# Optimization experiments

Measured on AMD Instinct MI355X. Metric: run time of the kernel, lower is better.

The kernel has to match this reference:

```python
import jax, jax.numpy as jnp
import numpy as np

M_FUZZ = 2.0        # self.m
EPSILON = 1e-8      # self.Epsilon
MAX_ITER = 25       # self.max_iterion


def setup_inputs() -> dict:
    key = jax.random.key(0)
    k1, k2 = jax.random.split(key)
    data = jax.random.normal(k1, (300000, 64), dtype=jnp.float32)
    u0_raw = jax.random.uniform(k2, (300000, 64), dtype=jnp.float32)
    return {"data": data, "u0_raw": u0_raw, "cluster": 64}


def reference(data, u0_raw, cluster):
    # Fuzzy c-means, faithful to GranularComputing.forward:
    #   iterate: C = center(U); U = update(U, C); C_new = center(U);
    #            stop if ||C_new - C||_F < Epsilon; return C (pre-update center).
    m = M_FUZZ
    p = 2.0 / (m - 1.0)  # exponent in membership update (== 2.0)
    N, D = data.shape

    # initialize_matrix_U: random rows normalized to sum to 1
    U0 = u0_raw / jnp.sum(u0_raw, axis=1, keepdims=True)  # [N, c]

    def center(U):
        Um = U ** m                                        # [N, c]
        num = Um.T @ data                                  # [c, D]
        den = jnp.sum(Um, axis=0)[:, None]                 # [c, 1]
        return num / den

    x2 = jnp.sum(data * data, axis=1, keepdims=True)       # [N, 1]

    def sqdist(C):
        # squared Euclidean distances [N, c] via expansion (no N x c x D tensor)
        c2 = jnp.sum(C * C, axis=1)                        # [c]
        return jnp.maximum(x2 + c2 - 2.0 * (data @ C.T), 0.0)

    def step(carry, _):
        U, C_ret, done = carry
        C = center(U)                                      # [c, D]
        # u_ij = 1 / sum_k (d_ij / d_ik)^p  ==  d_ij^{-p} / sum_k d_ik^{-p}
        w = sqdist(C) ** (-p / 2.0)                        # [N, c]
        U_new = w / jnp.sum(w, axis=1, keepdims=True)
        C_new = center(U_new)
        diff = jnp.sqrt(jnp.sum((C_new - C) ** 2))
        # freeze state after convergence (emulates the early break)
        U_out = jnp.where(done, U, U_new)
        C_out = jnp.where(done, C_ret, C)
        return (U_out, C_out, done | (diff < EPSILON)), None

    C0 = jnp.zeros((cluster, D), dtype=data.dtype)
    (_, V, _), _ = jax.lax.scan(
        step, (U0, C0, jnp.array(False)), None, length=MAX_ITER + 1
    )
    return V  # [cluster, D]
```

## Files before the change

### kernel.cpp

```cpp
#include <hip/hip_runtime.h>


#define DM 64
#define CL 64
#define PARTIAL_STRIDE 4160
#define MAX_ITER 25
#define MAX_BLOCKS 768
#define LDP 72

typedef __attribute__((ext_vector_type(8))) short bf16x8;
typedef __attribute__((ext_vector_type(4))) float f32x4;

__device__ __forceinline__ unsigned f2bf1(float f) {
  unsigned u = __builtin_bit_cast(unsigned, f);
  return (u + 0x7FFFu + ((u >> 16) & 1u)) >> 16;
}
__device__ __forceinline__ unsigned pkbf(float a, float b) {
  return f2bf1(a) | (f2bf1(b) << 16);
}
__device__ __forceinline__ unsigned cvtpk_bf16(float a, float b) {
  unsigned r;
  asm("v_cvt_pk_bf16_f32 %0, %1, %2" : "=v"(r) : "v"(a), "v"(b));
  return r;
}

__device__ __forceinline__ float wave_sum(float v) {
#define DPPADD(ctrl, rmask)                                                  \
  v += __builtin_bit_cast(float, __builtin_amdgcn_update_dpp(                \
           0, __builtin_bit_cast(int, v), ctrl, rmask, 0xf, false));
  DPPADD(0x111, 0xf)
  DPPADD(0x112, 0xf)
  DPPADD(0x114, 0xf)
  DPPADD(0x118, 0xf)
  DPPADD(0x142, 0xa)
  DPPADD(0x143, 0xc)
#undef DPPADD
  return __builtin_bit_cast(
      float, __builtin_amdgcn_readlane(__builtin_bit_cast(int, v), 63));
}

__device__ __forceinline__ float group16_sum(float v) {
#define DPPADD(ctrl)                                                         \
  v += __builtin_bit_cast(float, __builtin_amdgcn_update_dpp(                \
           0, __builtin_bit_cast(int, v), ctrl, 0xf, 0xf, false));
  DPPADD(0xB1)
  DPPADD(0x4E)
  DPPADD(0x141)
  DPPADD(0x140)
#undef DPPADD
  return v;
}

__global__ __launch_bounds__(256)
void fcm_prep(const float* __restrict__ data, float* __restrict__ x2,
              unsigned short* __restrict__ xbf,
              float* __restrict__ diffac, int* __restrict__ done,
              int* __restrict__ ticket, int N) {
  size_t i = (size_t)blockIdx.x * blockDim.x + threadIdx.x;
  if (i == 0) { *diffac = 0.0f; *done = 0; *ticket = 0; }
  size_t nvec = (size_t)N * (DM / 4);
  if (i >= nvec) return;
  float4 v = ((const float4*)data)[i];
  float s = fmaf(v.x, v.x, fmaf(v.y, v.y, fmaf(v.z, v.z, v.w * v.w)));
  float rs = group16_sum(s);
  if ((threadIdx.x & 15) == 0) x2[i >> 4] = rs;
  uint2 pk = {cvtpk_bf16(v.x, v.y), cvtpk_bf16(v.z, v.w)};
  ((uint2*)xbf)[i] = pk;
}

template <bool INIT>
__global__ __launch_bounds__(256, 3)
void fcm_pass(const unsigned short* __restrict__ xbf, const float* __restrict__ x2,
              const float* __restrict__ CU,
              float* __restrict__ partial, const int* __restrict__ done,
              int N, int ntiles) {
  if (!INIT && *done) return;
  __shared__ __align__(16) unsigned short Xb[2][64 * LDP];
  __shared__ __align__(16) unsigned short XTb[2][64 * LDP];
  __shared__ __align__(16) unsigned short umT[64 * LDP];
  __shared__ __align__(16) float x2s[2][64];

  const int tid  = threadIdx.x;
  const int w    = __builtin_amdgcn_readfirstlane(tid >> 6);
  const int col  = tid & 15;
  const int quad = (tid >> 4) & 3;

  bf16x8 cf0[4], cf1[4];
  float c2v[4];
  if (!INIT) {
#pragma unroll
    for (int jt = 0; jt < 4; jt++) {
      const float* crow = CU + (size_t)(16 * jt + col) * DM;
      float4 ca = *(const float4*)(crow + quad * 8);
      float4 cb = *(const float4*)(crow + quad * 8 + 4);
      float4 cc = *(const float4*)(crow + 32 + quad * 8);
      float4 cd = *(const float4*)(crow + 32 + quad * 8 + 4);
      float cp = ca.x*ca.x + ca.y*ca.y + ca.z*ca.z + ca.w*ca.w
               + cb.x*cb.x + cb.y*cb.y + cb.z*cb.z + cb.w*cb.w
               + cc.x*cc.x + cc.y*cc.y + cc.z*cc.z + cc.w*cc.w
               + cd.x*cd.x + cd.y*cd.y + cd.z*cd.z + cd.w*cd.w;
      cp += __shfl_xor(cp, 16, 64);
      cp += __shfl_xor(cp, 32, 64);
      c2v[jt] = cp;
      union { bf16x8 v; unsigned u[4]; } P0, P1;
      P0.u[0] = pkbf(ca.x, ca.y); P0.u[1] = pkbf(ca.z, ca.w);
      P0.u[2] = pkbf(cb.x, cb.y); P0.u[3] = pkbf(cb.z, cb.w);
      P1.u[0] = pkbf(cc.x, cc.y); P1.u[1] = pkbf(cc.z, cc.w);
      P1.u[2] = pkbf(cd.x, cd.y); P1.u[3] = pkbf(cd.z, cd.w);
      cf0[jt] = P0.v; cf1[jt] = P1.v;
    }
  }

  union { bf16x8 v; unsigned u[4]; } ON;
  ON.u[0] = ON.u[1] = ON.u[2] = ON.u[3] = 0x3F803F80u;
  const bf16x8 onesf = ON.v;

  f32x4 D2[4];
#pragma unroll
  for (int dt = 0; dt < 4; dt++) D2[dt] = f32x4{0.f, 0.f, 0.f, 0.f};
  f32x4 Dden = f32x4{0.f, 0.f, 0.f, 0.f};

  const int sp  = tid & 63;
  const int sd0 = (tid >> 6) * 8;
  const unsigned short* gsrc = xbf + (size_t)sp * DM + sd0;

  auto do_gemm2 = [&](int cb) {
#pragma unroll
    for (int pb = 0; pb < 2; pb++) {
      bf16x8 au = *(const bf16x8*)(const void*)&umT[(16 * w + col) * LDP + pb * 32 + quad * 8];
      Dden = __builtin_amdgcn_mfma_f32_16x16x32_bf16(au, onesf, Dden, 0, 0, 0);
#pragma unroll
      for (int dt = 0; dt < 4; dt++) {
        bf16x8 bx = *(const bf16x8*)(const void*)&XTb[cb][(dt * 16 + col) * LDP + pb * 32 + quad * 8];
        D2[dt] = __builtin_amdgcn_mfma_f32_16x16x32_bf16(au, bx, D2[dt], 0, 0, 0);
      }
    }
  };

  bf16x8 rv0 = {0, 0, 0, 0, 0, 0, 0, 0};
  bf16x8 rv1 = {0, 0, 0, 0, 0, 0, 0, 0};
  float rx2 = 0.0f;
  {
    int t0 = blockIdx.x;
    if (t0 < ntiles) {
      int base = t0 * 64;
      int np = min(64, N - base);
      if (sp < np) {
        const unsigned short* g = gsrc + (size_t)base * DM;
        rv0 = *(const bf16x8*)(g);
        rv1 = *(const bf16x8*)(g + 32);
      }
      if (tid < 64 && base + tid < N) rx2 = x2[base + tid];
    }
  }

  int c = 0;
  int it = 0;
  for (int t = blockIdx.x; t < ntiles; t += gridDim.x, ++it) {
    const int base = t * 64;
    const int np = min(64, N - base);
    __syncthreads();

    if (it > 0) do_gemm2(c ^ 1);

    *(bf16x8*)(void*)&Xb[c][sp * LDP + sd0] = rv0;
    *(bf16x8*)(void*)&Xb[c][sp * LDP + sd0 + 32] = rv1;
#pragma unroll
    for (int k = 0; k < 8; k++) XTb[c][(sd0 + k) * LDP + sp] = (unsigned short)rv0[k];
#pragma unroll
    for (int k = 0; k < 8; k++) XTb[c][(sd0 + 32 + k) * LDP + sp] = (unsigned short)rv1[k];
    if (tid < 64) x2s[c][tid] = rx2;

    {
      int tn = t + gridDim.x;
      rv0 = bf16x8{0, 0, 0, 0, 0, 0, 0, 0};
      rv1 = bf16x8{0, 0, 0, 0, 0, 0, 0, 0};
      rx2 = 0.0f;
      if (tn < ntiles) {
        int nbase = tn * 64;
        int nnp = min(64, N - nbase);
        if (sp < nnp) {
          const unsigned short* g = gsrc + (size_t)nbase * DM;
          rv0 = *(const bf16x8*)(g);
          rv1 = *(const bf16x8*)(g + 32);
        }
        if (tid < 64 && nbase + tid < N) rx2 = x2[nbase + tid];
      }
    }
    __syncthreads();

    float Wv[4][4];
    if (INIT) {
#pragma unroll
      for (int jt = 0; jt < 4; jt++)
#pragma unroll
        for (int r = 0; r < 4; r++) {
          int pl = 16 * w + quad * 4 + r;
          Wv[jt][r] = (pl < np)
              ? CU[(size_t)(base + pl) * CL + 16 * jt + col] : 0.0f;
        }
    } else {
      bf16x8 a0 = *(const bf16x8*)(const void*)&Xb[c][(16 * w + col) * LDP + quad * 8];
      bf16x8 a1 = *(const bf16x8*)(const void*)&Xb[c][(16 * w + col) * LDP + 32 + quad * 8];
      f32x4 x2p = *(const f32x4*)(const void*)&x2s[c][16 * w + quad * 4];
#pragma unroll
      for (int jt = 0; jt < 4; jt++) {
        f32x4 s = f32x4{0.f, 0.f, 0.f, 0.f};
        s = __builtin_amdgcn_mfma_f32_16x16x32_bf16(a0, cf0[jt], s, 0, 0, 0);
        s = __builtin_amdgcn_mfma_f32_16x16x32_bf16(a1, cf1[jt], s, 0, 0, 0);
#pragma unroll
        for (int r = 0; r < 4; r++) {
          float dist = fmaxf(fmaf(-2.0f, s[r], x2p[r] + c2v[jt]), 0.0f);
          Wv[jt][r] = __builtin_amdgcn_rcpf(dist);
        }
      }
    }

    float rr[4];
#pragma unroll
    for (int r = 0; r < 4; r++) {
      float rs = Wv[0][r] + Wv[1][r] + Wv[2][r] + Wv[3][r];
      rs = group16_sum(rs);
      int pl = 16 * w + quad * 4 + r;
      rr[r] = (pl < np) ? __builtin_amdgcn_rcpf(rs) : 0.0f;
    }

#pragma unroll
    for (int jt = 0; jt < 4; jt++) {
      float u0v = Wv[jt][0] * rr[0], u1v = Wv[jt][1] * rr[1];
      float u2v = Wv[jt][2] * rr[2], u3v = Wv[jt][3] * rr[3];
      uint2 pk = {cvtpk_bf16(u0v * u0v, u1v * u1v),
                  cvtpk_bf16(u2v * u2v, u3v * u3v)};
      *(uint2*)(void*)&umT[(16 * jt + col) * LDP + 16 * w + quad * 4] = pk;
    }
    c ^= 1;
  }

  if (it > 0) {
    __syncthreads();
    do_gemm2(c ^ 1);
  }

  float* pbuf = partial + (size_t)blockIdx.x * PARTIAL_STRIDE;
  if (col == 0) {
    float4 dv = {Dden[0], Dden[1], Dden[2], Dden[3]};
    *(float4*)(void*)&pbuf[CL * DM + 16 * w + quad * 4] = dv;
  }
#pragma unroll
  for (int dt = 0; dt < 4; dt++)
#pragma unroll
    for (int r = 0; r < 4; r++)
      pbuf[(size_t)(16 * w + quad * 4 + r) * DM + dt * 16 + col] = D2[dt][r];
}

__global__ __launch_bounds__(1024, 1)
void fcm_reduce(const float* __restrict__ partial, float* __restrict__ Cnew,
                const float* __restrict__ Cold, float* __restrict__ out,
                float* __restrict__ diffac, int* __restrict__ done,
                int* __restrict__ ticket, int compute_diff, int nb) {
  if (compute_diff && *done) return;
  __shared__ float sm[16 * 64];
  __shared__ float sden[1024];
  __shared__ int lastflag;
  __shared__ float sdiff;
  int j = blockIdx.x;
  int tid = threadIdx.x;
  int d = tid & 63;
  int slice = tid >> 6;
  float s = 0.0f;
  for (int b = slice; b < nb; b += 16)
    s += partial[(size_t)b * PARTIAL_STRIDE + j * DM + d];
  sm[slice * 64 + d] = s;
  float dv = 0.0f;
  for (int b = tid; b < nb; b += 1024)
    dv += partial[(size_t)b * PARTIAL_STRIDE + CL * DM + j];
  sden[tid] = dv;
  __syncthreads();
#pragma unroll
  for (int st = 8; st; st >>= 1) {
    if (slice < st) sm[slice * 64 + d] += sm[(slice + st) * 64 + d];
    __syncthreads();
  }
#pragma unroll
  for (int st = 512; st >= 64; st >>= 1) {
    if (tid < st) sden[tid] += sden[tid + st];
    __syncthreads();
  }
  if (tid < 64) {
    float denj = wave_sum(sden[tid]);
    float c = sm[tid] / denj;
    Cnew[j * DM + tid] = c;
    if (compute_diff) {
      float df = c - Cold[j * DM + tid];
      float tot = wave_sum(df * df);
      if (tid == 0) atomicAdd(diffac, tot);
    }
  }
  if (!compute_diff) return;
  __syncthreads();
  if (tid == 0) {
    __threadfence();
    int t = atomicAdd(ticket, 1);
    lastflag = (t == (int)gridDim.x - 1);
  }
  __syncthreads();
  if (!lastflag) return;
  if (tid == 0) sdiff = atomicAdd(diffac, 0.0f);
  __syncthreads();
  if (sdiff < 1e-16f) {
    for (int i = tid; i < CL * DM; i += 1024) out[i] = Cold[i];
    if (tid == 0) *done = 1;
  }
  if (tid == 0) { *diffac = 0.0f; *ticket = 0; }
}

__global__ void fcm_final(const float* __restrict__ Clast, float* __restrict__ out,
                          const int* __restrict__ done) {
  if (*done) return;
  int i = blockIdx.x * blockDim.x + threadIdx.x;
  if (i < CL * DM) out[i] = Clast[i];
}

extern "C" void kernel_launch(void* const* d_in, const int* in_sizes, int n_in,
                              void* d_out, int out_size, void* d_ws, size_t ws_size,
                              hipStream_t stream) {
  const float* data = (const float*)d_in[0];
  const float* u0   = (const float*)d_in[1];
  float* out = (float*)d_out;
  int N = in_sizes[0] / DM;
  int ntiles = (N + 63) / 64;

  float* ws = (float*)d_ws;
  size_t Noff = ((size_t)N + 15) & ~(size_t)15;
  float* x2 = ws;
  unsigned short* xbf = (unsigned short*)(ws + Noff);
  float* C0 = ws + Noff + (size_t)N * 32;
  float* C1 = C0 + CL * DM;
  float* diffac = C1 + CL * DM;
  int* done = (int*)(diffac + 1);
  int* ticket = (int*)(diffac + 2);
  float* partial = diffac + 16;

  size_t used = Noff + (size_t)N * 32 + 2 * CL * DM + 16;
  size_t avail = (ws_size / 4 > used) ? (ws_size / 4 - used) / PARTIAL_STRIDE : 0;
  int nb = (int)(avail < MAX_BLOCKS ? avail : MAX_BLOCKS);
  if (nb < 1) nb = 1;

  size_t nvec = (size_t)N * (DM / 4);
  hipLaunchKernelGGL(fcm_prep, dim3((unsigned)((nvec + 255) / 256)), dim3(256), 0,
                     stream, data, x2, xbf, diffac, done, ticket, N);
  hipLaunchKernelGGL((fcm_pass<true>), dim3(nb), dim3(256), 0, stream,
                     xbf, x2, u0, partial, done, N, ntiles);
  hipLaunchKernelGGL(fcm_reduce, dim3(64), dim3(1024), 0, stream,
                     partial, C0, C1, out, diffac, done, ticket, 0, nb);

  float* bufs[2] = {C0, C1};
  for (int k = 0; k < MAX_ITER; k++) {
    float* Cc = bufs[k & 1];
    float* Cn = bufs[(k + 1) & 1];
    hipLaunchKernelGGL((fcm_pass<false>), dim3(nb), dim3(256), 0, stream,
                       xbf, x2, Cc, partial, done, N, ntiles);
    hipLaunchKernelGGL(fcm_reduce, dim3(64), dim3(1024), 0, stream,
                       partial, Cn, Cc, out, diffac, done, ticket, 1, nb);
  }
  hipLaunchKernelGGL(fcm_final, dim3(16), dim3(256), 0, stream,
                     bufs[1], out, done);
}
```

Before: 379.0 us.

## Fuse per-iteration center reduction into the pass kernel with a grid spin barrier

```diff
diff --git a/kernel.cpp b/kernel.cpp
--- a/kernel.cpp
+++ b/kernel.cpp
@@ -55,9 +55,9 @@
 void fcm_prep(const float* __restrict__ data, float* __restrict__ x2,
               unsigned short* __restrict__ xbf,
               float* __restrict__ diffac, int* __restrict__ done,
-              int* __restrict__ ticket, int N) {
+              int* __restrict__ ticket, int* __restrict__ rdone, int N) {
   size_t i = (size_t)blockIdx.x * blockDim.x + threadIdx.x;
-  if (i == 0) { *diffac = 0.0f; *done = 0; *ticket = 0; }
+  if (i == 0) { *diffac = 0.0f; *done = 0; *ticket = 0; *rdone = 0; }
   size_t nvec = (size_t)N * (DM / 4);
   if (i >= nvec) return;
   float4 v = ((const float4*)data)[i];
@@ -68,74 +68,156 @@
   ((uint2*)xbf)[i] = pk;
 }
 
-template <bool INIT>
 __global__ __launch_bounds__(256, 3)
-void fcm_pass(const unsigned short* __restrict__ xbf, const float* __restrict__ x2,
-              const float* __restrict__ CU,
-              float* __restrict__ partial, const int* __restrict__ done,
-              int N, int ntiles) {
-  if (!INIT && *done) return;
+void fcm_pass_init(const unsigned short* __restrict__ xbf,
+                   const float* __restrict__ CU,
+                   float* __restrict__ partial, int N, int ntiles) {
+  __shared__ __align__(16) unsigned short Xb[2][64 * LDP];
+  __shared__ __align__(16) unsigned short XTb[2][64 * LDP];
+  __shared__ __align__(16) unsigned short umT[64 * LDP];
+
+  const int tid  = threadIdx.x;
+  const int w    = __builtin_amdgcn_readfirstlane(tid >> 6);
+  const int col  = tid & 15;
+  const int quad = (tid >> 4) & 3;
+
+  union { bf16x8 v; unsigned u[4]; } ON;
+  ON.u[0] = ON.u[1] = ON.u[2] = ON.u[3] = 0x3F803F80u;
+  const bf16x8 onesf = ON.v;
+
+  f32x4 D2[4];
+#pragma unroll
+  for (int dt = 0; dt < 4; dt++) D2[dt] = f32x4{0.f, 0.f, 0.f, 0.f};
+  f32x4 Dden = f32x4{0.f, 0.f, 0.f, 0.f};
+
+  const int sp  = tid & 63;
+  const int sd0 = (tid >> 6) * 8;
+  const unsigned short* gsrc = xbf + (size_t)sp * DM + sd0;
+
+  auto do_gemm2 = [&](int cb) {
+#pragma unroll
+    for (int pb = 0; pb < 2; pb++) {
+      bf16x8 au = *(const bf16x8*)(const void*)&umT[(16 * w + col) * LDP + pb * 32 + quad * 8];
+      Dden = __builtin_amdgcn_mfma_f32_16x16x32_bf16(au, onesf, Dden, 0, 0, 0);
+#pragma unroll
+      for (int dt = 0; dt < 4; dt++) {
+        bf16x8 bx = *(const bf16x8*)(const void*)&XTb[cb][(dt * 16 + col) * LDP + pb * 32 + quad * 8];
+        D2[dt] = __builtin_amdgcn_mfma_f32_16x16x32_bf16(au, bx, D2[dt], 0, 0, 0);
+      }
+    }
+  };
+
+  bf16x8 rv0 = {0, 0, 0, 0, 0, 0, 0, 0};
+  bf16x8 rv1 = {0, 0, 0, 0, 0, 0, 0, 0};
+  {
+    int t0 = blockIdx.x;
+    if (t0 < ntiles) {
+      int base = t0 * 64;
+      int np = min(64, N - base);
+      if (sp < np) {
+        const unsigned short* g = gsrc + (size_t)base * DM;
+        rv0 = *(const bf16x8*)(g);
+        rv1 = *(const bf16x8*)(g + 32);
+      }
+    }
+  }
+
+  int c = 0, it = 0;
+  for (int t = blockIdx.x; t < ntiles; t += gridDim.x, ++it) {
+    const int base = t * 64;
+    const int np = min(64, N - base);
+    __syncthreads();
+    if (it > 0) do_gemm2(c ^ 1);
+
+    *(bf16x8*)(void*)&Xb[c][sp * LDP + sd0] = rv0;
+    *(bf16x8*)(void*)&Xb[c][sp * LDP + sd0 + 32] = rv1;
+#pragma unroll
+    for (int k = 0; k < 8; k++) XTb[c][(sd0 + k) * LDP + sp] = (unsigned short)rv0[k];
+#pragma unroll
+    for (int k = 0; k < 8; k++) XTb[c][(sd0 + 32 + k) * LDP + sp] = (unsigned short)rv1[k];
+
+    {
+      int tn = t + gridDim.x;
+      rv0 = bf16x8{0, 0, 0, 0, 0, 0, 0, 0};
+      rv1 = bf16x8{0, 0, 0, 0, 0, 0, 0, 0};
+      if (tn < ntiles) {
+        int nbase = tn * 64;
+        int nnp = min(64, N - nbase);
+        if (sp < nnp) {
+          const unsigned short* g = gsrc + (size_t)nbase * DM;
+          rv0 = *(const bf16x8*)(g);
+          rv1 = *(const bf16x8*)(g + 32);
+        }
+      }
+    }
+    __syncthreads();
+
+    float Wv[4][4];
+#pragma unroll
+    for (int jt = 0; jt < 4; jt++)
+#pragma unroll
+      for (int r = 0; r < 4; r++) {
+        int pl = 16 * w + quad * 4 + r;
+        Wv[jt][r] = (pl < np)
+            ? CU[(size_t)(base + pl) * CL + 16 * jt + col] : 0.0f;
+      }
+
+    float rr[4];
+#pragma unroll
+    for (int r = 0; r < 4; r++) {
+      float rs = Wv[0][r] + Wv[1][r] + Wv[2][r] + Wv[3][r];
+      rs = group16_sum(rs);
+      int pl = 16 * w + quad * 4 + r;
+      rr[r] = (pl < np) ? __builtin_amdgcn_rcpf(rs) : 0.0f;
+    }
+
+#pragma unroll
+    for (int jt = 0; jt < 4; jt++) {
+      float u0v = Wv[jt][0] * rr[0], u1v = Wv[jt][1] * rr[1];
+      float u2v = Wv[jt][2] * rr[2], u3v = Wv[jt][3] * rr[3];
+      uint2 pk = {cvtpk_bf16(u0v * u0v, u1v * u1v),
+                  cvtpk_bf16(u2v * u2v, u3v * u3v)};
+      *(uint2*)(void*)&umT[(16 * jt + col) * LDP + 16 * w + quad * 4] = pk;
+    }
+    c ^= 1;
+  }
+  if (it > 0) { __syncthreads(); do_gemm2(c ^ 1); }
+
+  float* pbuf = partial + (size_t)blockIdx.x * PARTIAL_STRIDE;
+  if (col == 0) {
+    float4 dv = {Dden[0], Dden[1], Dden[2], Dden[3]};
+    *(float4*)(void*)&pbuf[CL * DM + 16 * w + quad * 4] = dv;
+  }
+#pragma unroll
+  for (int dt = 0; dt < 4; dt++)
+#pragma unroll
+    for (int r = 0; r < 4; r++)
+      pbuf[(size_t)(16 * w + quad * 4 + r) * DM + dt * 16 + col] = D2[dt][r];
+}
+
+__global__ __launch_bounds__(256, 3)
+void fcm_iter(const unsigned short* __restrict__ xbf, const float* __restrict__ x2,
+              float* __restrict__ Cnew, const float* __restrict__ Cold,
+              float* __restrict__ partial, float* __restrict__ out,
+              float* __restrict__ diffac, int* __restrict__ done,
+              int* __restrict__ ticket, int* __restrict__ rdone,
+              int k, int N, int ntiles, int nb) {
+  if (*done) return;
   __shared__ __align__(16) unsigned short Xb[2][64 * LDP];
   __shared__ __align__(16) unsigned short XTb[2][64 * LDP];
   __shared__ __align__(16) unsigned short umT[64 * LDP];
   __shared__ __align__(16) float x2s[2][64];
+  __shared__ int s_lastflag;
+  __shared__ float s_sdiff;
 
   const int tid  = threadIdx.x;
   const int w    = __builtin_amdgcn_readfirstlane(tid >> 6);
   const int col  = tid & 15;
   const int quad = (tid >> 4) & 3;
 
-  bf16x8 cf0[4], cf1[4];
-  float c2v[4];
-  if (!INIT) {
-#pragma unroll
-    for (int jt = 0; jt < 4; jt++) {
-      const float* crow = CU + (size_t)(16 * jt + col) * DM;
-      float4 ca = *(const float4*)(crow + quad * 8);
-      float4 cb = *(const float4*)(crow + quad * 8 + 4);
-      float4 cc = *(const float4*)(crow + 32 + quad * 8);
-      float4 cd = *(const float4*)(crow + 32 + quad * 8 + 4);
-      float cp = ca.x*ca.x + ca.y*ca.y + ca.z*ca.z + ca.w*ca.w
-               + cb.x*cb.x + cb.y*cb.y + cb.z*cb.z + cb.w*cb.w
-               + cc.x*cc.x + cc.y*cc.y + cc.z*cc.z + cc.w*cc.w
-               + cd.x*cd.x + cd.y*cd.y + cd.z*cd.z + cd.w*cd.w;
-      cp += __shfl_xor(cp, 16, 64);
-      cp += __shfl_xor(cp, 32, 64);
-      c2v[jt] = cp;
-      union { bf16x8 v; unsigned u[4]; } P0, P1;
-      P0.u[0] = pkbf(ca.x, ca.y); P0.u[1] = pkbf(ca.z, ca.w);
-      P0.u[2] = pkbf(cb.x, cb.y); P0.u[3] = pkbf(cb.z, cb.w);
-      P1.u[0] = pkbf(cc.x, cc.y); P1.u[1] = pkbf(cc.z, cc.w);
-      P1.u[2] = pkbf(cd.x, cd.y); P1.u[3] = pkbf(cd.z, cd.w);
-      cf0[jt] = P0.v; cf1[jt] = P1.v;
-    }
-  }
-
-  union { bf16x8 v; unsigned u[4]; } ON;
-  ON.u[0] = ON.u[1] = ON.u[2] = ON.u[3] = 0x3F803F80u;
-  const bf16x8 onesf = ON.v;
-
-  f32x4 D2[4];
-#pragma unroll
-  for (int dt = 0; dt < 4; dt++) D2[dt] = f32x4{0.f, 0.f, 0.f, 0.f};
-  f32x4 Dden = f32x4{0.f, 0.f, 0.f, 0.f};
-
   const int sp  = tid & 63;
   const int sd0 = (tid >> 6) * 8;
   const unsigned short* gsrc = xbf + (size_t)sp * DM + sd0;
-
-  auto do_gemm2 = [&](int cb) {
-#pragma unroll
-    for (int pb = 0; pb < 2; pb++) {
-      bf16x8 au = *(const bf16x8*)(const void*)&umT[(16 * w + col) * LDP + pb * 32 + quad * 8];
-      Dden = __builtin_amdgcn_mfma_f32_16x16x32_bf16(au, onesf, Dden, 0, 0, 0);
-#pragma unroll
-      for (int dt = 0; dt < 4; dt++) {
-        bf16x8 bx = *(const bf16x8*)(const void*)&XTb[cb][(dt * 16 + col) * LDP + pb * 32 + quad * 8];
-        D2[dt] = __builtin_amdgcn_mfma_f32_16x16x32_bf16(au, bx, D2[dt], 0, 0, 0);
-      }
-    }
-  };
 
   bf16x8 rv0 = {0, 0, 0, 0, 0, 0, 0, 0};
   bf16x8 rv1 = {0, 0, 0, 0, 0, 0, 0, 0};
@@ -154,21 +236,123 @@
     }
   }
 
-  int c = 0;
-  int it = 0;
+  if (blockIdx.x < 64) {
+    const int j = blockIdx.x;
+    float* red  = (float*)&Xb[0][0];
+    float* sden = red + 256;
+    const int d = tid & 63;
+    const int slice = tid >> 6;
+    float s = 0.0f;
+    for (int b = slice; b < nb; b += 4)
+      s += partial[(size_t)b * PARTIAL_STRIDE + j * DM + d];
+    red[slice * 64 + d] = s;
+    float dv = 0.0f;
+    for (int b = tid; b < nb; b += 256)
+      dv += partial[(size_t)b * PARTIAL_STRIDE + CL * DM + j];
+    sden[tid] = dv;
+    __syncthreads();
+    if (tid < 128) sden[tid] += sden[tid + 128];
+    __syncthreads();
+    if (tid < 64) sden[tid] += sden[tid + 64];
+    __syncthreads();
+    if (tid < 64) {
+      float denj = wave_sum(sden[tid]);
+      float cs = red[tid] + red[64 + tid] + red[128 + tid] + red[192 + tid];
+      float cval = cs / denj;
+      Cnew[j * DM + tid] = cval;
+      if (k > 0) {
+        float df = cval - Cold[j * DM + tid];
+        float tot = wave_sum(df * df);
+        if (tid == 0) atomicAdd(diffac, tot);
+      }
+    }
+    __threadfence();
+    if (k > 0) {
+      if (tid == 0) s_lastflag = (atomicAdd(ticket, 1) == CL - 1);
+      __syncthreads();
+      if (s_lastflag) {
+        if (tid == 0) s_sdiff = atomicAdd(diffac, 0.0f);
+        __syncthreads();
+        if (s_sdiff < 1e-16f) {
+          for (int i = tid; i < CL * DM; i += 256) out[i] = Cold[i];
+          if (tid == 0) *done = 1;
+        }
+        if (tid == 0) { *diffac = 0.0f; *ticket = 0; }
+        __threadfence();
+      }
+    }
+    __syncthreads();
+    if (tid == 0) { __threadfence(); atomicAdd(rdone, 1); }
+  }
+
+  if (tid == 0) {
+    while (__hip_atomic_load(rdone, __ATOMIC_RELAXED,
+                             __HIP_MEMORY_SCOPE_AGENT) < 64 * (k + 1))
+      __builtin_amdgcn_s_sleep(8);
+  }
+  __syncthreads();
+  __threadfence();
+  if (__hip_atomic_load(done, __ATOMIC_RELAXED, __HIP_MEMORY_SCOPE_AGENT)) return;
+
+  bf16x8 cf0[4], cf1[4];
+  float c2v[4];
+#pragma unroll
+  for (int jt = 0; jt < 4; jt++) {
+    const float* crow = Cnew + (size_t)(16 * jt + col) * DM;
+    float4 ca = *(const float4*)(crow + quad * 8);
+    float4 cb = *(const float4*)(crow + quad * 8 + 4);
+    float4 cc = *(const float4*)(crow + 32 + quad * 8);
+    float4 cd = *(const float4*)(crow + 32 + quad * 8 + 4);
+    float cp = ca.x*ca.x + ca.y*ca.y + ca.z*ca.z + ca.w*ca.w
+             + cb.x*cb.x + cb.y*cb.y + cb.z*cb.z + cb.w*cb.w
+             + cc.x*cc.x + cc.y*cc.y + cc.z*cc.z + cc.w*cc.w
+             + cd.x*cd.x + cd.y*cd.y + cd.z*cd.z + cd.w*cd.w;
+    cp += __shfl_xor(cp, 16, 64);
+    cp += __shfl_xor(cp, 32, 64);
+    c2v[jt] = cp;
+    union { bf16x8 v; unsigned u[4]; } P0, P1;
+    P0.u[0] = pkbf(ca.x, ca.y); P0.u[1] = pkbf(ca.z, ca.w);
+    P0.u[2] = pkbf(cb.x, cb.y); P0.u[3] = pkbf(cb.z, cb.w);
+    P1.u[0] = pkbf(cc.x, cc.y); P1.u[1] = pkbf(cc.z, cc.w);
+    P1.u[2] = pkbf(cd.x, cd.y); P1.u[3] = pkbf(cd.z, cd.w);
+    cf0[jt] = P0.v; cf1[jt] = P1.v;
+  }
+
+  union { bf16x8 v; unsigned u[4]; } ON;
+  ON.u[0] = ON.u[1] = ON.u[2] = ON.u[3] = 0x3F803F80u;
+  const bf16x8 onesf = ON.v;
+
+  f32x4 D2[4];
+#pragma unroll
+  for (int dt = 0; dt < 4; dt++) D2[dt] = f32x4{0.f, 0.f, 0.f, 0.f};
+  f32x4 Dden = f32x4{0.f, 0.f, 0.f, 0.f};
+
+  auto do_gemm2 = [&](int cb) {
+#pragma unroll
+    for (int pb = 0; pb < 2; pb++) {
+      bf16x8 au = *(const bf16x8*)(const void*)&umT[(16 * w + col) * LDP + pb * 32 + quad * 8];
+      Dden = __builtin_amdgcn_mfma_f32_16x16x32_bf16(au, onesf, Dden, 0, 0, 0);
+#pragma unroll
+      for (int dt = 0; dt < 4; dt++) {
+        bf16x8 bx = *(const bf16x8*)(const void*)&XTb[cb][(dt * 16 + col) * LDP + pb * 32 + quad * 8];
+        D2[dt] = __builtin_amdgcn_mfma_f32_16x16x32_bf16(au, bx, D2[dt], 0, 0, 0);
+      }
+    }
+  };
+
+  int c = 0, it = 0;
   for (int t = blockIdx.x; t < ntiles; t += gridDim.x, ++it) {
     const int base = t * 64;
     const int np = min(64, N - base);
     __syncthreads();
-
     if (it > 0) do_gemm2(c ^ 1);
 
     *(bf16x8*)(void*)&Xb[c][sp * LDP + sd0] = rv0;
     *(bf16x8*)(void*)&Xb[c][sp * LDP + sd0 + 32] = rv1;
 #pragma unroll
-    for (int k = 0; k < 8; k++) XTb[c][(sd0 + k) * LDP + sp] = (unsigned short)rv0[k];
-#pragma unroll
-    for (int k = 0; k < 8; k++) XTb[c][(sd0 + 32 + k) * LDP + sp] = (unsigned short)rv1[k];
+    for (int q = 0; q < 8; q++) XTb[c][(sd0 + q) * LDP + sp] = (unsigned short)rv0[q];
+#pragma unroll
+    for (int q = 0; q < 8; q++) XTb[c][(sd0 + 32 + q) * LDP + sp] = (unsigned short)rv1[q];
     if (tid < 64) x2s[c][tid] = rx2;
 
     {
@@ -190,16 +374,7 @@
     __syncthreads();
 
     float Wv[4][4];
-    if (INIT) {
-#pragma unroll
-      for (int jt = 0; jt < 4; jt++)
-#pragma unroll
-        for (int r = 0; r < 4; r++) {
-          int pl = 16 * w + quad * 4 + r;
-          Wv[jt][r] = (pl < np)
-              ? CU[(size_t)(base + pl) * CL + 16 * jt + col] : 0.0f;
-        }
-    } else {
+    {
       bf16x8 a0 = *(const bf16x8*)(const void*)&Xb[c][(16 * w + col) * LDP + quad * 8];
       bf16x8 a1 = *(const bf16x8*)(const void*)&Xb[c][(16 * w + col) * LDP + 32 + quad * 8];
       f32x4 x2p = *(const f32x4*)(const void*)&x2s[c][16 * w + quad * 4];
@@ -235,11 +410,7 @@
     }
     c ^= 1;
   }
-
-  if (it > 0) {
-    __syncthreads();
-    do_gemm2(c ^ 1);
-  }
+  if (it > 0) { __syncthreads(); do_gemm2(c ^ 1); }
 
   float* pbuf = partial + (size_t)blockIdx.x * PARTIAL_STRIDE;
   if (col == 0) {
@@ -339,30 +510,30 @@
   float* diffac = C1 + CL * DM;
   int* done = (int*)(diffac + 1);
   int* ticket = (int*)(diffac + 2);
+  int* rdone = (int*)(diffac + 3);
   float* partial = diffac + 16;
 
   size_t used = Noff + (size_t)N * 32 + 2 * CL * DM + 16;
   size_t avail = (ws_size / 4 > used) ? (ws_size / 4 - used) / PARTIAL_STRIDE : 0;
   int nb = (int)(avail < MAX_BLOCKS ? avail : MAX_BLOCKS);
-  if (nb < 1) nb = 1;
+  if (nb < 64) nb = 64;
 
   size_t nvec = (size_t)N * (DM / 4);
   hipLaunchKernelGGL(fcm_prep, dim3((unsigned)((nvec + 255) / 256)), dim3(256), 0,
-                     stream, data, x2, xbf, diffac, done, ticket, N);
-  hipLaunchKernelGGL((fcm_pass<true>), dim3(nb), dim3(256), 0, stream,
-                     xbf, x2, u0, partial, done, N, ntiles);
-  hipLaunchKernelGGL(fcm_reduce, dim3(64), dim3(1024), 0, stream,
-                     partial, C0, C1, out, diffac, done, ticket, 0, nb);
+                     stream, data, x2, xbf, diffac, done, ticket, rdone, N);
+  hipLaunchKernelGGL(fcm_pass_init, dim3(nb), dim3(256), 0, stream,
+                     xbf, u0, partial, N, ntiles);
 
   float* bufs[2] = {C0, C1};
   for (int k = 0; k < MAX_ITER; k++) {
-    float* Cc = bufs[k & 1];
-    float* Cn = bufs[(k + 1) & 1];
-    hipLaunchKernelGGL((fcm_pass<false>), dim3(nb), dim3(256), 0, stream,
-                       xbf, x2, Cc, partial, done, N, ntiles);
-    hipLaunchKernelGGL(fcm_reduce, dim3(64), dim3(1024), 0, stream,
-                       partial, Cn, Cc, out, diffac, done, ticket, 1, nb);
-  }
+    float* Cn = bufs[k & 1];
+    float* Co = bufs[(k + 1) & 1];
+    hipLaunchKernelGGL(fcm_iter, dim3(nb), dim3(256), 0, stream,
+                       xbf, x2, Cn, Co, partial, out, diffac, done, ticket,
+                       rdone, k, N, ntiles, nb);
+  }
+  hipLaunchKernelGGL(fcm_reduce, dim3(64), dim3(1024), 0, stream,
+                     partial, bufs[1], bufs[0], out, diffac, done, ticket, 1, nb);
   hipLaunchKernelGGL(fcm_final, dim3(16), dim3(256), 0, stream,
                      bufs[1], out, done);
 }
```

Measured after the change: 754.2 us. 99.0% more time.
